# Kernel tuning notes

Measured on AMD Instinct MI355X. Metric: run time of the kernel, lower is better.

The kernel has to match this reference:

```python
import jax, jax.numpy as jnp
import numpy as np
import math

K = 10  # args.k, hardcoded in order_topk/fast_topk

def sinusoid_pe(seq_len, d_model, dtype=jnp.float32):
    # PositionalEmbedding: pe[:,0::2]=sin(pos*div), pe[:,1::2]=cos(pos*div)
    pos = jnp.arange(seq_len, dtype=jnp.float32)[:, None]
    div = jnp.exp(jnp.arange(0, d_model, 2, dtype=jnp.float32) * (-math.log(10000.0) / d_model))
    ang = pos * div  # [S, d_model//2]
    pe = jnp.zeros((seq_len, d_model), dtype=jnp.float32)
    pe = pe.at[:, 0::2].set(jnp.sin(ang)).at[:, 1::2].set(jnp.cos(ang))
    return pe.astype(dtype)


def setup_inputs() -> dict:
    key = jax.random.key(0)
    ks = jax.random.split(key, 5)
    B, D, S = 128, 512, 512
    scale1 = 1.0 / math.sqrt(2 * D)
    scale2 = 1.0 / math.sqrt(D)
    return {
        "x": jax.random.normal(ks[0], (B, D, S), dtype=jnp.float32),
        "w1": jax.random.normal(ks[1], (2 * D, D), dtype=jnp.float32) * scale1,
        "b1": jax.random.normal(ks[2], (D,), dtype=jnp.float32) * scale1,
        "w2": jax.random.normal(ks[3], (D, 1), dtype=jnp.float32) * scale2,
        "b2": jax.random.normal(ks[4], (1,), dtype=jnp.float32) * scale2,
    }


def reference(x, w1, b1, w2, b2):
    # x: [B, D, S] -> feature: [B, S, D]  (Sampler: x = x.transpose(-1,-2))
    feat = jnp.swapaxes(x, -1, -2)
    B, S, D = feat.shape
    # shot == 1 branch: per-video mean over tokens, broadcast over seq
    info_g = jnp.broadcast_to(feat.mean(axis=-2, keepdims=True), feat.shape)
    h = jnp.concatenate([feat, info_g], axis=-1)  # [B, S, 2D]
    # evaluator: PositionalEmbedding(1024) -> Linear(1024,512) -> ReLU -> Linear(512,1)
    h = h + sinusoid_pe(S, 2 * D, h.dtype)[None]
    score = jax.nn.relu(jnp.einsum('bsf,fd->bsd', h, w1) + b1)
    score = (jnp.einsum('bsd,do->bso', score, w2) + b2)[..., 0]  # [B, S]
    mn = score.min(axis=1, keepdims=True)
    mx = score.max(axis=1, keepdims=True)
    norm_score = (score - mn) / (mx - mn + 1e-4)
    # fast_topk (eval path): top-k indices, sorted ascending, one-hot selection
    _, idx = jax.lax.top_k(norm_score, K)      # [B, K]
    idx = jnp.sort(idx, axis=-1)
    # torch: one_hot -> [B,K,S], .transpose(-1,-2) -> [B,S,K], then indices.transpose(-1,-2) -> [B,K,S]
    indices = jax.nn.one_hot(idx, S, dtype=feat.dtype)  # [B, K, S]
    selected_feature = jnp.einsum('bks,bsd->bkd', indices, feat)  # bmm gather
    return indices, selected_feature, feat
```

## Files before the change

kernel.cpp:

```cpp
#include <hip/hip_runtime.h>
#include <math.h>

#define B 128
#define D 512
#define S 512
#define TOPK 10

typedef short bf16x8 __attribute__((ext_vector_type(8)));
typedef float f32x4 __attribute__((ext_vector_type(4)));
typedef short short4v __attribute__((ext_vector_type(4)));


__global__ void zero_kernel(float* __restrict__ p) {
    p[blockIdx.x * 256 + threadIdx.x] = 0.0f;
}

__global__ __launch_bounds__(256) void transpose_mean_kernel(
    const float* __restrict__ x, float* __restrict__ feat, float* __restrict__ g) {
    __shared__ float tile[64 * 65];
    int b = blockIdx.z;
    int s0 = blockIdx.x * 64, d0 = blockIdx.y * 64;
    int t = threadIdx.x;
    int ty = t >> 4, tx = t & 15;
    const float4* x4 = (const float4*)(x + (size_t)b * D * S);
    float psum[4];
#pragma unroll
    for (int q = 0; q < 4; ++q) {
        int d = ty + 16 * q;
        float4 v = x4[(size_t)(d0 + d) * (S / 4) + (s0 >> 2) + tx];
        tile[d + (4 * tx + 0) * 65] = v.x;
        tile[d + (4 * tx + 1) * 65] = v.y;
        tile[d + (4 * tx + 2) * 65] = v.z;
        tile[d + (4 * tx + 3) * 65] = v.w;
        float sm = (v.x + v.y) + (v.z + v.w);
#pragma unroll
        for (int off = 8; off; off >>= 1) sm += __shfl_down(sm, off, 16);
        psum[q] = sm;
    }
    if (tx == 0) {
#pragma unroll
        for (int q = 0; q < 4; ++q)
            atomicAdd(&g[b * D + d0 + ty + 16 * q], psum[q] * (1.0f / S));
    }
    __syncthreads();
    float4* f4 = (float4*)(feat + (size_t)b * S * D);
#pragma unroll
    for (int q = 0; q < 4; ++q) {
        int s = ty + 16 * q;
        float4 o;
        o.x = tile[(4 * tx + 0) + s * 65];
        o.y = tile[(4 * tx + 1) + s * 65];
        o.z = tile[(4 * tx + 2) + s * 65];
        o.w = tile[(4 * tx + 3) + s * 65];
        f4[(size_t)(s0 + s) * (D / 4) + (d0 >> 2) + tx] = o;
    }
}

__device__ __forceinline__ unsigned splitf(float f) {
    unsigned u = __float_as_uint(f);
    unsigned rb = u + 0x7FFFu + ((u >> 16) & 1u);
    float hf = __uint_as_float(rb & 0xFFFF0000u);
    unsigned u2 = __float_as_uint(f - hf);
    return (rb >> 16) | (u2 & 0xFFFF0000u);
}

__global__ void pe_kernel(ushort* __restrict__ peh, ushort* __restrict__ pel) {
    int s = blockIdx.x, t = threadIdx.x;
#pragma unroll
    for (int q = 0; q < 2; ++q) {
        int i = t + 256 * q;
        float ei = expf((float)(2 * i) * -0.0089944730195f);
        float ang = (float)s * ei;
        float sv = sinf(ang), cv = cosf(ang);
        unsigned ps = splitf(sv), pc = splitf(cv);
        size_t base = (size_t)s * 1024 + 2 * i;
        peh[base] = (ushort)(ps & 0xFFFFu);
        peh[base + 1] = (ushort)(pc & 0xFFFFu);
        pel[base] = (ushort)(ps >> 16);
        pel[base + 1] = (ushort)(pc >> 16);
    }
}

__global__ void w1split_kernel(const float* __restrict__ w1, ushort* __restrict__ w1th,
                               ushort* __restrict__ w1tl) {
    __shared__ float tile[32][33];
    int k0 = blockIdx.x * 32, d0 = blockIdx.y * 32;
    int tx = threadIdx.x, ty = threadIdx.y;
#pragma unroll
    for (int j = 0; j < 4; ++j)
        tile[ty + j * 8][tx] = w1[(size_t)(k0 + ty + j * 8) * D + d0 + tx];
    __syncthreads();
#pragma unroll
    for (int j = 0; j < 4; ++j) {
        unsigned p = splitf(tile[tx][ty + j * 8]);
        size_t idx = (size_t)(d0 + ty + j * 8) * 1024 + k0 + tx;
        w1th[idx] = (ushort)(p & 0xFFFFu);
        w1tl[idx] = (ushort)(p >> 16);
    }
}

#define CP 40
__global__ __launch_bounds__(256) void c1_mfma(
    const ushort* __restrict__ peh, const ushort* __restrict__ pel,
    const ushort* __restrict__ w1th, const ushort* __restrict__ w1tl,
    const float* __restrict__ b1, float* __restrict__ C1) {
    __shared__ short sAh[64 * CP];
    __shared__ short sAl[64 * CP];
    __shared__ short sBh[64 * CP];
    __shared__ short sBl[64 * CP];
    int t = threadIdx.x;
    int d0 = blockIdx.x * 64, s0 = blockIdx.y * 64;
    int w = t >> 6, l = t & 63, lc = l & 15, lg = l >> 4;
    int tm = t >> 2, tk = (t & 3) * 8;
    f32x4 acc[4] = {};
    for (int k0 = 0; k0 < 1024; k0 += 32) {
        __syncthreads();
        *(bf16x8*)(sAh + tm * CP + tk) = *(const bf16x8*)(peh + (size_t)(s0 + tm) * 1024 + k0 + tk);
        *(bf16x8*)(sAl + tm * CP + tk) = *(const bf16x8*)(pel + (size_t)(s0 + tm) * 1024 + k0 + tk);
        *(bf16x8*)(sBh + tm * CP + tk) = *(const bf16x8*)(w1th + (size_t)(d0 + tm) * 1024 + k0 + tk);
        *(bf16x8*)(sBl + tm * CP + tk) = *(const bf16x8*)(w1tl + (size_t)(d0 + tm) * 1024 + k0 + tk);
        __syncthreads();
        int m = w * 16 + lc;
        bf16x8 ah = *(const bf16x8*)(sAh + m * CP + lg * 8);
        bf16x8 al = *(const bf16x8*)(sAl + m * CP + lg * 8);
#pragma unroll
        for (int j = 0; j < 4; ++j) {
            int n = j * 16 + lc;
            bf16x8 bh = *(const bf16x8*)(sBh + n * CP + lg * 8);
            bf16x8 bl = *(const bf16x8*)(sBl + n * CP + lg * 8);
            acc[j] = __builtin_amdgcn_mfma_f32_16x16x32_bf16(ah, bh, acc[j], 0, 0, 0);
            acc[j] = __builtin_amdgcn_mfma_f32_16x16x32_bf16(ah, bl, acc[j], 0, 0, 0);
            acc[j] = __builtin_amdgcn_mfma_f32_16x16x32_bf16(al, bh, acc[j], 0, 0, 0);
        }
    }
#pragma unroll
    for (int j = 0; j < 4; ++j)
#pragma unroll
        for (int reg = 0; reg < 4; ++reg) {
            int sg = s0 + w * 16 + lg * 4 + reg;
            int dg = d0 + j * 16 + lc;
            C1[(size_t)sg * D + dg] = acc[j][reg] + b1[dg];
        }
}

__global__ void gterm_kernel(const float* __restrict__ g, const float* __restrict__ w1,
                             float* __restrict__ gterm) {
    int b = blockIdx.x;
    int d = blockIdx.y * 256 + threadIdx.x;
    int kc = blockIdx.z * 128;
    const float* gb = g + b * D + kc;
    float a0 = 0.f, a1 = 0.f, a2 = 0.f, a3 = 0.f;
    for (int k = 0; k < 128; k += 4) {
        a0 += gb[k + 0] * w1[(size_t)(D + kc + k + 0) * D + d];
        a1 += gb[k + 1] * w1[(size_t)(D + kc + k + 1) * D + d];
        a2 += gb[k + 2] * w1[(size_t)(D + kc + k + 2) * D + d];
        a3 += gb[k + 3] * w1[(size_t)(D + kc + k + 3) * D + d];
    }
    atomicAdd(&gterm[b * D + d], (a0 + a1) + (a2 + a3));
}

#define GP 40
__global__ __launch_bounds__(256, 2) void gemm_mfma(
    const float* __restrict__ feat, const ushort* __restrict__ w1th,
    const ushort* __restrict__ w1tl, const float* __restrict__ w2,
    const float* __restrict__ gterm, const float* __restrict__ C1,
    float* __restrict__ score) {
    __shared__ short sAh[128 * GP];
    __shared__ short sAl[128 * GP];
    __shared__ short sBh[128 * GP];
    __shared__ short sBl[128 * GP];
    int t = threadIdx.x;
    int d0 = blockIdx.x * 128;
    int row0 = blockIdx.y * 128;
    int b = row0 >> 9;
    int tm = t >> 3, tk4 = t & 7;
    int w = t >> 6, l = t & 63;
    int wr = w >> 1, wc = w & 1;
    int lc = l & 15, lg = l >> 4;

    f32x4 acc[4][4] = {};

    for (int k0 = 0; k0 < D; k0 += 32) {
        __syncthreads();
#pragma unroll
        for (int q = 0; q < 4; ++q) {
            int m = tm + 32 * q;
            const float4 v = *(const float4*)(feat + (size_t)(row0 + m) * D + k0 + tk4 * 4);
            unsigned p0 = splitf(v.x), p1 = splitf(v.y), p2 = splitf(v.z), p3 = splitf(v.w);
            short4v hi, lo;
            hi[0] = (short)(p0 & 0xFFFFu); lo[0] = (short)(p0 >> 16);
            hi[1] = (short)(p1 & 0xFFFFu); lo[1] = (short)(p1 >> 16);
            hi[2] = (short)(p2 & 0xFFFFu); lo[2] = (short)(p2 >> 16);
            hi[3] = (short)(p3 & 0xFFFFu); lo[3] = (short)(p3 >> 16);
            *(short4v*)(sAh + m * GP + tk4 * 4) = hi;
            *(short4v*)(sAl + m * GP + tk4 * 4) = lo;
            size_t widx = (size_t)(d0 + m) * 1024 + k0 + tk4 * 4;
            *(short4v*)(sBh + m * GP + tk4 * 4) = *(const short4v*)(w1th + widx);
            *(short4v*)(sBl + m * GP + tk4 * 4) = *(const short4v*)(w1tl + widx);
        }
        __syncthreads();
        bf16x8 ah[4], al[4], bh[4], bl[4];
#pragma unroll
        for (int i = 0; i < 4; ++i) {
            int m = wr * 64 + i * 16 + lc;
            ah[i] = *(const bf16x8*)(sAh + m * GP + lg * 8);
            al[i] = *(const bf16x8*)(sAl + m * GP + lg * 8);
            int n = wc * 64 + i * 16 + lc;
            bh[i] = *(const bf16x8*)(sBh + n * GP + lg * 8);
            bl[i] = *(const bf16x8*)(sBl + n * GP + lg * 8);
        }
#pragma unroll
        for (int i = 0; i < 4; ++i)
#pragma unroll
            for (int j = 0; j < 4; ++j) {
                acc[i][j] = __builtin_amdgcn_mfma_f32_16x16x32_bf16(ah[i], bh[j], acc[i][j], 0, 0, 0);
                acc[i][j] = __builtin_amdgcn_mfma_f32_16x16x32_bf16(ah[i], bl[j], acc[i][j], 0, 0, 0);
                acc[i][j] = __builtin_amdgcn_mfma_f32_16x16x32_bf16(al[i], bh[j], acc[i][j], 0, 0, 0);
            }
    }
    float w2v[4], gt[4];
#pragma unroll
    for (int j = 0; j < 4; ++j) {
        int d = d0 + wc * 64 + j * 16 + lc;
        w2v[j] = w2[d];
        gt[j] = gterm[b * D + d];
    }
#pragma unroll
    for (int i = 0; i < 4; ++i)
#pragma unroll
        for (int reg = 0; reg < 4; ++reg) {
            int srow = row0 + wr * 64 + i * 16 + lg * 4 + reg;
            int s = srow & 511;
            float part = 0.f;
#pragma unroll
            for (int j = 0; j < 4; ++j) {
                int d = d0 + wc * 64 + j * 16 + lc;
                float z = acc[i][j][reg] + gt[j] + C1[(size_t)s * D + d];
                part += w2v[j] * fmaxf(z, 0.f);
            }
#pragma unroll
            for (int off = 8; off; off >>= 1) part += __shfl_down(part, off, 16);
            if (lc == 0) atomicAdd(&score[srow], part);
        }
}

__global__ void topk_kernel(const float* __restrict__ score, const float* __restrict__ feat,
                            float* __restrict__ out_ind, float* __restrict__ out_sel) {
    __shared__ float work[512];
    __shared__ float wv[8];
    __shared__ int wi[8];
    __shared__ int topi[TOPK];
    int b = blockIdx.x, t = threadIdx.x;
    work[t] = score[b * S + t];
    __syncthreads();
    for (int it = 0; it < TOPK; ++it) {
        float v = work[t];
        int i = t;
#pragma unroll
        for (int off = 32; off; off >>= 1) {
            float ov = __shfl_down(v, off);
            int oi = __shfl_down(i, off);
            if (ov > v || (ov == v && oi < i)) { v = ov; i = oi; }
        }
        if ((t & 63) == 0) { wv[t >> 6] = v; wi[t >> 6] = i; }
        __syncthreads();
        if (t == 0) {
            float bv = wv[0];
            int bi = wi[0];
            for (int w = 1; w < 8; ++w)
                if (wv[w] > bv || (wv[w] == bv && wi[w] < bi)) { bv = wv[w]; bi = wi[w]; }
            topi[it] = bi;
            work[bi] = -INFINITY;
        }
        __syncthreads();
    }
    if (t == 0) {
        for (int a = 1; a < TOPK; ++a) {
            int key = topi[a];
            int c = a - 1;
            while (c >= 0 && topi[c] > key) { topi[c + 1] = topi[c]; --c; }
            topi[c + 1] = key;
        }
    }
    __syncthreads();
    float* oi_b = out_ind + (size_t)b * TOPK * S;
#pragma unroll
    for (int k = 0; k < TOPK; ++k) oi_b[k * S + t] = 0.0f;
    __syncthreads();
    if (t < TOPK) oi_b[t * S + topi[t]] = 1.0f;
    float* os_b = out_sel + (size_t)b * TOPK * D;
    const float* fb = feat + (size_t)b * S * D;
#pragma unroll
    for (int k = 0; k < TOPK; ++k) os_b[k * D + t] = fb[(size_t)topi[k] * D + t];
}

extern "C" void kernel_launch(void* const* d_in, const int* in_sizes, int n_in,
                              void* d_out, int out_size, void* d_ws, size_t ws_size,
                              hipStream_t stream) {
    const float* x  = (const float*)d_in[0];
    const float* w1 = (const float*)d_in[1];
    const float* b1 = (const float*)d_in[2];
    const float* w2 = (const float*)d_in[3];

    float* out = (float*)d_out;
    float* out_ind = out;
    float* out_sel = out + (size_t)B * TOPK * S;
    float* feat    = out + 2 * (size_t)B * TOPK * S;

    float* ws     = (float*)d_ws;
    float* g      = ws;
    float* gterm  = ws + 65536;
    float* score  = ws + 131072;
    float* C1     = ws + 196608;
    ushort* w1th  = (ushort*)(ws + 458752);
    ushort* w1tl  = (ushort*)(ws + 720896);
    ushort* peh   = (ushort*)(ws + 983040);
    ushort* pel   = (ushort*)(ws + 1245184);

    zero_kernel<<<768, 256, 0, stream>>>(ws);
    transpose_mean_kernel<<<dim3(8, 8, B), 256, 0, stream>>>(x, feat, g);
    gterm_kernel<<<dim3(B, 2, 4), 256, 0, stream>>>(g, w1, gterm);
    pe_kernel<<<S, 256, 0, stream>>>(peh, pel);
    w1split_kernel<<<dim3(32, 16), dim3(32, 8), 0, stream>>>(w1, w1th, w1tl);
    c1_mfma<<<dim3(8, 8), 256, 0, stream>>>(peh, pel, w1th, w1tl, b1, C1);
    gemm_mfma<<<dim3(4, 512), 256, 0, stream>>>(feat, w1th, w1tl, w2, gterm, C1, score);
    topk_kernel<<<B, 512, 0, stream>>>(score, feat, out_ind, out_sel);
}
```

Baseline: 437.9 us.

## Double-buffer main GEMM with swizzled hi/lo W1 layout and direct-to-LDS loads

Repacks the bf16 hi/lo split of W1 into one interleaved, tile-swizzled buffer so each 16-byte chunk holds hi and lo for eight k values. The main GEMM now uses 256x256 tiles with 512 threads, double-buffered LDS, and global_load_lds for the B operand. The feat loads for the next k-step are issued before the MFMAs and split after them, overlapping memory with compute. It also adds a block-index remap for locality. The cost is more registers per thread (32 accumulators), a larger LDS footprint, and fewer blocks.

```diff
diff --git a/kernel.cpp b/kernel.cpp
--- a/kernel.cpp
+++ b/kernel.cpp
@@ -7,6 +7,7 @@
 #define TOPK 10
 
 typedef short bf16x8 __attribute__((ext_vector_type(8)));
+typedef unsigned short u16x8 __attribute__((ext_vector_type(8)));
 typedef float f32x4 __attribute__((ext_vector_type(4)));
 typedef short short4v __attribute__((ext_vector_type(4)));
 
@@ -62,6 +63,11 @@
     float hf = __uint_as_float(rb & 0xFFFF0000u);
     unsigned u2 = __float_as_uint(f - hf);
     return (rb >> 16) | (u2 & 0xFFFF0000u);
+}
+
+__device__ __forceinline__ size_t w1t_off(int d, int k) {
+    return (size_t)(((d >> 8) * 32 + (k >> 5)) * 4 + ((k >> 3) & 3)) * 4096 +
+           (size_t)(d & 255) * 16 + (k & 7);
 }
 
 __global__ void pe_kernel(ushort* __restrict__ peh, ushort* __restrict__ pel) {
@@ -81,29 +87,31 @@
     }
 }
 
-__global__ void w1split_kernel(const float* __restrict__ w1, ushort* __restrict__ w1th,
-                               ushort* __restrict__ w1tl) {
-    __shared__ float tile[32][33];
-    int k0 = blockIdx.x * 32, d0 = blockIdx.y * 32;
-    int tx = threadIdx.x, ty = threadIdx.y;
-#pragma unroll
-    for (int j = 0; j < 4; ++j)
-        tile[ty + j * 8][tx] = w1[(size_t)(k0 + ty + j * 8) * D + d0 + tx];
-    __syncthreads();
-#pragma unroll
-    for (int j = 0; j < 4; ++j) {
-        unsigned p = splitf(tile[tx][ty + j * 8]);
-        size_t idx = (size_t)(d0 + ty + j * 8) * 1024 + k0 + tx;
-        w1th[idx] = (ushort)(p & 0xFFFFu);
-        w1tl[idx] = (ushort)(p >> 16);
+__global__ void w1split_kernel(const float* __restrict__ w1, ushort* __restrict__ w1tsw) {
+    int rp = blockIdx.x;
+    int tt = blockIdx.y;
+    int m = threadIdx.x;
+    int d = rp * 256 + m;
+    ushort* out = w1tsw + (size_t)(rp * 32 + tt) * 16384 + (size_t)m * 16;
+#pragma unroll
+    for (int c = 0; c < 4; ++c) {
+        u16x8 hi, lo;
+#pragma unroll
+        for (int j = 0; j < 8; ++j) {
+            unsigned p = splitf(w1[(size_t)(tt * 32 + c * 8 + j) * D + d]);
+            hi[j] = (ushort)(p & 0xFFFFu);
+            lo[j] = (ushort)(p >> 16);
+        }
+        *(u16x8*)(out + c * 4096) = hi;
+        *(u16x8*)(out + c * 4096 + 8) = lo;
     }
 }
 
 #define CP 40
 __global__ __launch_bounds__(256) void c1_mfma(
     const ushort* __restrict__ peh, const ushort* __restrict__ pel,
-    const ushort* __restrict__ w1th, const ushort* __restrict__ w1tl,
-    const float* __restrict__ b1, float* __restrict__ C1) {
+    const ushort* __restrict__ w1tsw, const float* __restrict__ b1,
+    float* __restrict__ C1) {
     __shared__ short sAh[64 * CP];
     __shared__ short sAl[64 * CP];
     __shared__ short sBh[64 * CP];
@@ -117,8 +125,9 @@
         __syncthreads();
         *(bf16x8*)(sAh + tm * CP + tk) = *(const bf16x8*)(peh + (size_t)(s0 + tm) * 1024 + k0 + tk);
         *(bf16x8*)(sAl + tm * CP + tk) = *(const bf16x8*)(pel + (size_t)(s0 + tm) * 1024 + k0 + tk);
-        *(bf16x8*)(sBh + tm * CP + tk) = *(const bf16x8*)(w1th + (size_t)(d0 + tm) * 1024 + k0 + tk);
-        *(bf16x8*)(sBl + tm * CP + tk) = *(const bf16x8*)(w1tl + (size_t)(d0 + tm) * 1024 + k0 + tk);
+        size_t boff = w1t_off(d0 + tm, k0 + tk);
+        *(bf16x8*)(sBh + tm * CP + tk) = *(const bf16x8*)(w1tsw + boff);
+        *(bf16x8*)(sBl + tm * CP + tk) = *(const bf16x8*)(w1tsw + boff + 8);
         __syncthreads();
         int m = w * 16 + lc;
         bf16x8 ah = *(const bf16x8*)(sAh + m * CP + lg * 8);
@@ -159,69 +168,113 @@
     atomicAdd(&gterm[b * D + d], (a0 + a1) + (a2 + a3));
 }
 
-#define GP 40
-__global__ __launch_bounds__(256, 2) void gemm_mfma(
-    const float* __restrict__ feat, const ushort* __restrict__ w1th,
-    const ushort* __restrict__ w1tl, const float* __restrict__ w2,
-    const float* __restrict__ gterm, const float* __restrict__ C1,
-    float* __restrict__ score) {
-    __shared__ short sAh[128 * GP];
-    __shared__ short sAl[128 * GP];
-    __shared__ short sBh[128 * GP];
-    __shared__ short sBl[128 * GP];
+__device__ __forceinline__ void gload16(const void* src, void* dst) {
+    __builtin_amdgcn_global_load_lds((const __attribute__((address_space(1))) void*)src,
+                                     (__attribute__((address_space(3))) void*)dst, 16, 0, 0);
+}
+
+__device__ __forceinline__ void split_write(short* sAbuf, int am, int ahalf,
+                                            float4 a0, float4 a1, float4 a2, float4 a3) {
+#pragma unroll
+    for (int cc = 0; cc < 2; ++cc) {
+        float e0, e1, e2, e3, e4, e5, e6, e7;
+        if (cc == 0) {
+            e0 = a0.x; e1 = a0.y; e2 = a0.z; e3 = a0.w;
+            e4 = a1.x; e5 = a1.y; e6 = a1.z; e7 = a1.w;
+        } else {
+            e0 = a2.x; e1 = a2.y; e2 = a2.z; e3 = a2.w;
+            e4 = a3.x; e5 = a3.y; e6 = a3.z; e7 = a3.w;
+        }
+        unsigned p0 = splitf(e0), p1 = splitf(e1), p2 = splitf(e2), p3 = splitf(e3);
+        unsigned p4 = splitf(e4), p5 = splitf(e5), p6 = splitf(e6), p7 = splitf(e7);
+        u16x8 hi, lo;
+        hi[0] = (ushort)(p0 & 0xFFFFu); lo[0] = (ushort)(p0 >> 16);
+        hi[1] = (ushort)(p1 & 0xFFFFu); lo[1] = (ushort)(p1 >> 16);
+        hi[2] = (ushort)(p2 & 0xFFFFu); lo[2] = (ushort)(p2 >> 16);
+        hi[3] = (ushort)(p3 & 0xFFFFu); lo[3] = (ushort)(p3 >> 16);
+        hi[4] = (ushort)(p4 & 0xFFFFu); lo[4] = (ushort)(p4 >> 16);
+        hi[5] = (ushort)(p5 & 0xFFFFu); lo[5] = (ushort)(p5 >> 16);
+        hi[6] = (ushort)(p6 & 0xFFFFu); lo[6] = (ushort)(p6 >> 16);
+        hi[7] = (ushort)(p7 & 0xFFFFu); lo[7] = (ushort)(p7 >> 16);
+        short* dst = sAbuf + (size_t)(2 * ahalf + cc) * 4096 + (size_t)am * 16;
+        *(u16x8*)dst = hi;
+        *(u16x8*)(dst + 8) = lo;
+    }
+}
+
+__global__ __launch_bounds__(512, 2) void gemm_mfma(
+    const float* __restrict__ feat, const ushort* __restrict__ w1tsw,
+    const float* __restrict__ w2, const float* __restrict__ gterm,
+    const float* __restrict__ C1, float* __restrict__ score) {
+    __shared__ short sA[2][4][256][16];
+    __shared__ short sB[2][4][256][16];
     int t = threadIdx.x;
-    int d0 = blockIdx.x * 128;
-    int row0 = blockIdx.y * 128;
+    int id = (int)blockIdx.x;
+    int lid = (id & 7) * 64 + (id >> 3);
+    int rp = lid >> 1, cp = lid & 1;
+    int row0 = rp << 8;
+    int d0 = cp << 8;
     int b = row0 >> 9;
-    int tm = t >> 3, tk4 = t & 7;
-    int w = t >> 6, l = t & 63;
-    int wr = w >> 1, wc = w & 1;
-    int lc = l & 15, lg = l >> 4;
-
-    f32x4 acc[4][4] = {};
-
-    for (int k0 = 0; k0 < D; k0 += 32) {
-        __syncthreads();
-#pragma unroll
-        for (int q = 0; q < 4; ++q) {
-            int m = tm + 32 * q;
-            const float4 v = *(const float4*)(feat + (size_t)(row0 + m) * D + k0 + tk4 * 4);
-            unsigned p0 = splitf(v.x), p1 = splitf(v.y), p2 = splitf(v.z), p3 = splitf(v.w);
-            short4v hi, lo;
-            hi[0] = (short)(p0 & 0xFFFFu); lo[0] = (short)(p0 >> 16);
-            hi[1] = (short)(p1 & 0xFFFFu); lo[1] = (short)(p1 >> 16);
-            hi[2] = (short)(p2 & 0xFFFFu); lo[2] = (short)(p2 >> 16);
-            hi[3] = (short)(p3 & 0xFFFFu); lo[3] = (short)(p3 >> 16);
-            *(short4v*)(sAh + m * GP + tk4 * 4) = hi;
-            *(short4v*)(sAl + m * GP + tk4 * 4) = lo;
-            size_t widx = (size_t)(d0 + m) * 1024 + k0 + tk4 * 4;
-            *(short4v*)(sBh + m * GP + tk4 * 4) = *(const short4v*)(w1th + widx);
-            *(short4v*)(sBl + m * GP + tk4 * 4) = *(const short4v*)(w1tl + widx);
-        }
-        __syncthreads();
-        bf16x8 ah[4], al[4], bh[4], bl[4];
+
+    int am = t & 255, ahalf = t >> 8;
+    const float4* asrc = (const float4*)(feat + (size_t)(row0 + am) * D + ahalf * 16);
+    const ushort* btile = w1tsw + (size_t)(cp * 32) * 16384;
+    int wv = t >> 6, l = t & 63, lc = l & 15, lg = l >> 4;
+    int wr = wv >> 1, wc = wv & 1;
+    int wbase = (t & ~63);
+
+    f32x4 acc[4][8] = {};
+
+    {
+        float4 a0 = asrc[0], a1 = asrc[1], a2 = asrc[2], a3 = asrc[3];
+#pragma unroll
+        for (int q = 0; q < 4; ++q)
+            gload16(btile + (size_t)(q * 512 + t) * 8,
+                    &sB[0][0][0][0] + (size_t)(q * 512 + wbase) * 8);
+        split_write(&sA[0][0][0][0], am, ahalf, a0, a1, a2, a3);
+    }
+    __syncthreads();
+
+    for (int ts = 0; ts < 16; ++ts) {
+        int cur = ts & 1, nxt = cur ^ 1;
+        float4 a0, a1, a2, a3;
+        if (ts < 15) {
+            a0 = asrc[(ts + 1) * 8 + 0];
+            a1 = asrc[(ts + 1) * 8 + 1];
+            a2 = asrc[(ts + 1) * 8 + 2];
+            a3 = asrc[(ts + 1) * 8 + 3];
+#pragma unroll
+            for (int q = 0; q < 4; ++q)
+                gload16(btile + (size_t)(ts + 1) * 16384 + (size_t)(q * 512 + t) * 8,
+                        &sB[nxt][0][0][0] + (size_t)(q * 512 + wbase) * 8);
+        }
+        bf16x8 ahf[4], alf[4];
 #pragma unroll
         for (int i = 0; i < 4; ++i) {
-            int m = wr * 64 + i * 16 + lc;
-            ah[i] = *(const bf16x8*)(sAh + m * GP + lg * 8);
-            al[i] = *(const bf16x8*)(sAl + m * GP + lg * 8);
-            int n = wc * 64 + i * 16 + lc;
-            bh[i] = *(const bf16x8*)(sBh + n * GP + lg * 8);
-            bl[i] = *(const bf16x8*)(sBl + n * GP + lg * 8);
-        }
-#pragma unroll
-        for (int i = 0; i < 4; ++i)
-#pragma unroll
-            for (int j = 0; j < 4; ++j) {
-                acc[i][j] = __builtin_amdgcn_mfma_f32_16x16x32_bf16(ah[i], bh[j], acc[i][j], 0, 0, 0);
-                acc[i][j] = __builtin_amdgcn_mfma_f32_16x16x32_bf16(ah[i], bl[j], acc[i][j], 0, 0, 0);
-                acc[i][j] = __builtin_amdgcn_mfma_f32_16x16x32_bf16(al[i], bh[j], acc[i][j], 0, 0, 0);
+            const short* ap = &sA[cur][lg][wr * 64 + i * 16 + lc][0];
+            ahf[i] = *(const bf16x8*)(ap);
+            alf[i] = *(const bf16x8*)(ap + 8);
+        }
+#pragma unroll
+        for (int j = 0; j < 8; ++j) {
+            const short* bp = &sB[cur][lg][wc * 128 + j * 16 + lc][0];
+            bf16x8 bh = *(const bf16x8*)(bp);
+            bf16x8 bl = *(const bf16x8*)(bp + 8);
+#pragma unroll
+            for (int i = 0; i < 4; ++i) {
+                acc[i][j] = __builtin_amdgcn_mfma_f32_16x16x32_bf16(ahf[i], bh, acc[i][j], 0, 0, 0);
+                acc[i][j] = __builtin_amdgcn_mfma_f32_16x16x32_bf16(ahf[i], bl, acc[i][j], 0, 0, 0);
+                acc[i][j] = __builtin_amdgcn_mfma_f32_16x16x32_bf16(alf[i], bh, acc[i][j], 0, 0, 0);
             }
-    }
-    float w2v[4], gt[4];
-#pragma unroll
-    for (int j = 0; j < 4; ++j) {
-        int d = d0 + wc * 64 + j * 16 + lc;
+        }
+        if (ts < 15) split_write(&sA[nxt][0][0][0], am, ahalf, a0, a1, a2, a3);
+        __syncthreads();
+    }
+
+    float w2v[8], gt[8];
+#pragma unroll
+    for (int j = 0; j < 8; ++j) {
+        int d = d0 + wc * 128 + j * 16 + lc;
         w2v[j] = w2[d];
         gt[j] = gterm[b * D + d];
     }
@@ -233,8 +286,8 @@
             int s = srow & 511;
             float part = 0.f;
 #pragma unroll
-            for (int j = 0; j < 4; ++j) {
-                int d = d0 + wc * 64 + j * 16 + lc;
+            for (int j = 0; j < 8; ++j) {
+                int d = d0 + wc * 128 + j * 16 + lc;
                 float z = acc[i][j][reg] + gt[j] + C1[(size_t)s * D + d];
                 part += w2v[j] * fmaxf(z, 0.f);
             }
@@ -247,8 +300,8 @@
 __global__ void topk_kernel(const float* __restrict__ score, const float* __restrict__ feat,
                             float* __restrict__ out_ind, float* __restrict__ out_sel) {
     __shared__ float work[512];
-    __shared__ float wv[8];
-    __shared__ int wi[8];
+    __shared__ float wvv[8];
+    __shared__ int wii[8];
     __shared__ int topi[TOPK];
     int b = blockIdx.x, t = threadIdx.x;
     work[t] = score[b * S + t];
@@ -262,13 +315,13 @@
             int oi = __shfl_down(i, off);
             if (ov > v || (ov == v && oi < i)) { v = ov; i = oi; }
         }
-        if ((t & 63) == 0) { wv[t >> 6] = v; wi[t >> 6] = i; }
+        if ((t & 63) == 0) { wvv[t >> 6] = v; wii[t >> 6] = i; }
         __syncthreads();
         if (t == 0) {
-            float bv = wv[0];
-            int bi = wi[0];
+            float bv = wvv[0];
+            int bi = wii[0];
             for (int w = 1; w < 8; ++w)
-                if (wv[w] > bv || (wv[w] == bv && wi[w] < bi)) { bv = wv[w]; bi = wi[w]; }
+                if (wvv[w] > bv || (wvv[w] == bv && wii[w] < bi)) { bv = wvv[w]; bi = wii[w]; }
             topi[it] = bi;
             work[bi] = -INFINITY;
         }
@@ -307,22 +360,21 @@
     float* out_sel = out + (size_t)B * TOPK * S;
     float* feat    = out + 2 * (size_t)B * TOPK * S;
 
-    float* ws     = (float*)d_ws;
-    float* g      = ws;
-    float* gterm  = ws + 65536;
-    float* score  = ws + 131072;
-    float* C1     = ws + 196608;
-    ushort* w1th  = (ushort*)(ws + 458752);
-    ushort* w1tl  = (ushort*)(ws + 720896);
-    ushort* peh   = (ushort*)(ws + 983040);
-    ushort* pel   = (ushort*)(ws + 1245184);
+    float* ws      = (float*)d_ws;
+    float* g       = ws;
+    float* gterm   = ws + 65536;
+    float* score   = ws + 131072;
+    float* C1      = ws + 196608;
+    ushort* w1tsw  = (ushort*)(ws + 458752);
+    ushort* peh    = (ushort*)(ws + 983040);
+    ushort* pel    = (ushort*)(ws + 1245184);
 
     zero_kernel<<<768, 256, 0, stream>>>(ws);
     transpose_mean_kernel<<<dim3(8, 8, B), 256, 0, stream>>>(x, feat, g);
     gterm_kernel<<<dim3(B, 2, 4), 256, 0, stream>>>(g, w1, gterm);
     pe_kernel<<<S, 256, 0, stream>>>(peh, pel);
-    w1split_kernel<<<dim3(32, 16), dim3(32, 8), 0, stream>>>(w1, w1th, w1tl);
-    c1_mfma<<<dim3(8, 8), 256, 0, stream>>>(peh, pel, w1th, w1tl, b1, C1);
-    gemm_mfma<<<dim3(4, 512), 256, 0, stream>>>(feat, w1th, w1tl, w2, gterm, C1, score);
+    w1split_kernel<<<dim3(2, 32), 256, 0, stream>>>(w1, w1tsw);
+    c1_mfma<<<dim3(8, 8), 256, 0, stream>>>(peh, pel, w1tsw, b1, C1);
+    gemm_mfma<<<512, 512, 0, stream>>>(feat, w1tsw, w2, gterm, C1, score);
     topk_kernel<<<B, 512, 0, stream>>>(score, feat, out_ind, out_sel);
 }
```

Result: faster. 421.7 us (-3.7%).
